# Optimization experiments

Measured on AMD Instinct MI355X. Metric: run time of the kernel, lower is better.

## Reference

```python
import jax, jax.numpy as jnp
import numpy as np

# --- hyperparameters (match module defaults) ---
W_CLASSIFY = 1.1          # weight_factor_classify
W_SAMPLE = 1.0            # weight_factor_sample (mid weight add)
LOSS_WEIGHTS = (1.0, 1.0, 1.0)
PARAMS_HEAD = dict(a=80.0, b=1500.0, c=1750.0, d=2000.0, t=-0.5)
PARAMS_CHEST = dict(a=10.0, b=75.0, c=85.0, d=100.0, t=-0.5)
PARAMS_NECK = dict(a=0.15, b=1.5, c=1.7, d=1.9, t=-0.5)

# AIS thresholds (reimplemented in-kernel; original used numpy round-trips)
HEAD_THR = np.array([150.0, 500.0, 1000.0, 1800.0, 2600.0], dtype=np.float32)
CHEST_THR = np.array([22.0, 35.0, 45.0, 55.0, 65.0], dtype=np.float32)
CHEST_OT_SCALE = np.array([0.8, 0.9, 1.0, 1.1, 1.2], dtype=np.float32)  # per occupant-type
NECK_THR = np.array([0.2, 0.5, 1.0, 1.5, 2.0], dtype=np.float32)


def piecewise_linear(y_true, y_pred, p, mid):
    a, b, c, d, t = p['a'], p['b'], p['c'], p['d'], p['t']
    k = -np.log(t + 1.0) / d  # decay rate for y > d
    w = jnp.zeros_like(y_true)
    w = jnp.where((y_true >= 0) & (y_true < a), (mid / a) * y_true, w)
    w = jnp.where((y_true >= a) & (y_true <= b), mid, w)
    w = jnp.where((y_true > b) & (y_true < c), mid - (mid / (c - b)) * (y_true - b), w)
    w = jnp.where((y_true >= c) & (y_true <= d), 0.0, w)
    w = jnp.where(y_true > d, -1.0 + jnp.exp(-k * (y_true - d)), w)
    w = w + jnp.where(y_pred < 0, mid, 0.0)
    return w


def ais_from_thresholds(x, thr):
    # piecewise-constant AIS class: number of thresholds exceeded, in [0, 5]
    return jnp.sum(x[:, None] >= thr[None, :], axis=-1).astype(jnp.float32)


def task_loss(pred, true, ais_pred, ais_true, params):
    # AIS values are classification results of detached values in the
    # original (no grad) -> stop_gradient here.
    w_cls = W_CLASSIFY ** jnp.abs(jax.lax.stop_gradient(ais_pred) - jax.lax.stop_gradient(ais_true))
    w_mid = 1.0 + piecewise_linear(true, pred, params, W_SAMPLE)
    base = jnp.abs(pred - true)  # MAE, reduction='none'
    return jnp.mean(base * w_cls * w_mid)


def setup_inputs() -> dict:
    key = jax.random.key(0)
    k1, k2, k3 = jax.random.split(key, 3)
    B = 4194304
    scales = jnp.array([2500.0, 120.0, 2.5], dtype=jnp.float32)  # HIC, Dmax, Nij ranges
    pred = (jax.random.uniform(k1, (B, 3), dtype=jnp.float32) * 1.1 - 0.05) * scales
    true = jax.random.uniform(k2, (B, 3), dtype=jnp.float32) * scales
    ot = jax.random.randint(k3, (B,), 0, 5, dtype=jnp.int32)
    return {"pred": pred, "true": true, "ot": ot}


def reference(pred, true, ot):
    thr_head = jnp.asarray(HEAD_THR)
    thr_neck = jnp.asarray(NECK_THR)
    # chest thresholds scale with occupant type -> per-sample thresholds
    thr_chest = jnp.asarray(CHEST_THR)[None, :] * jnp.asarray(CHEST_OT_SCALE)[ot][:, None]

    p_hic, p_dmax, p_nij = pred[:, 0], pred[:, 1], pred[:, 2]
    t_hic, t_dmax, t_nij = true[:, 0], true[:, 1], true[:, 2]

    loss_hic = task_loss(p_hic, t_hic,
                         ais_from_thresholds(p_hic, thr_head),
                         ais_from_thresholds(t_hic, thr_head), PARAMS_HEAD)

    ais_p_chest = jnp.sum(p_dmax[:, None] >= thr_chest, axis=-1).astype(jnp.float32)
    ais_t_chest = jnp.sum(t_dmax[:, None] >= thr_chest, axis=-1).astype(jnp.float32)
    loss_dmax = task_loss(p_dmax, t_dmax, ais_p_chest, ais_t_chest, PARAMS_CHEST)

    loss_nij = task_loss(p_nij, t_nij,
                         ais_from_thresholds(p_nij, thr_neck),
                         ais_from_thresholds(t_nij, thr_neck), PARAMS_NECK)

    w_hic, w_dmax, w_nij = LOSS_WEIGHTS
    return w_hic * loss_hic + w_dmax * loss_dmax + w_nij * loss_nij
```

## Files before the change

### kernel.cpp

```cpp
#include <hip/hip_runtime.h>

#define NT 256
#define NB 1536

__device__ __forceinline__ float elem_loss(float p, float t, float se,
    float t0, float t1, float t2, float t3, float t4,
    float ainv, float bb, float cbinv, float dd, float dinv) {
    float u0 = t0 * se, u1 = t1 * se, u2 = t2 * se, u3 = t3 * se, u4 = t4 * se;
    int ap = (p >= u0) + (p >= u1) + (p >= u2) + (p >= u3) + (p >= u4);
    int at = (t >= u0) + (t >= u1) + (t >= u2) + (t >= u3) + (t >= u4);
    float wc = exp2f(fabsf((float)(ap - at)) * 0.13750352374993502f);
    float ramp = t * ainv;
    float down = 1.0f - (t - bb) * cbinv;
    float wm = fmaxf(fminf(fminf(ramp, 1.0f), down), 0.0f);
    float tail = exp2f((dd - t) * dinv) - 1.0f;
    wm = (t > dd) ? tail : wm;
    wm += (p < 0.0f) ? 2.0f : 1.0f;
    return fabsf(p - t) * wc * wm;
}

#define SEL0(x0, x1, x2) (c1 ? (x1) : (c2 ? (x2) : (x0)))
#define SEL1(x0, x1, x2) (c1 ? (x2) : (c2 ? (x0) : (x1)))
#define SEL2(x0, x1, x2) (c1 ? (x0) : (c2 ? (x1) : (x2)))

#define DECL_SLOT(n, SEL) \
    const float t0_##n = SEL(150.0f, 22.0f, 0.2f); \
    const float t1_##n = SEL(500.0f, 35.0f, 0.5f); \
    const float t2_##n = SEL(1000.0f, 45.0f, 1.0f); \
    const float t3_##n = SEL(1800.0f, 55.0f, 1.5f); \
    const float t4_##n = SEL(2600.0f, 65.0f, 2.0f); \
    const float ainv_##n = SEL(0.0125f, 0.1f, 6.6666667f); \
    const float bb_##n   = SEL(1500.0f, 75.0f, 1.5f); \
    const float cbinv_##n= SEL(0.004f, 0.1f, 5.0f); \
    const float dd_##n   = SEL(2000.0f, 100.0f, 1.9f); \
    const float dinv_##n = SEL(0.0005f, 0.01f, 0.52631579f); \
    const bool  ch_##n   = SEL(false, true, false);

#define SLOT_LOSS(n, p, t) \
    elem_loss((p), (t), ch_##n ? (off_##n ? s1 : s0) : 1.0f, \
              t0_##n, t1_##n, t2_##n, t3_##n, t4_##n, \
              ainv_##n, bb_##n, cbinv_##n, dd_##n, dinv_##n)

__global__ __launch_bounds__(NT)
void weighted_loss_main(const float* __restrict__ pred,
                        const float* __restrict__ truth,
                        const int*   __restrict__ ot,
                        float* __restrict__ partial, int B) {
    const int total  = 3 * B;
    const int nchunk = total >> 2;
    const int g = blockIdx.x * NT + threadIdx.x;
    const int S = gridDim.x * NT;

    const int  q  = g % 3;
    const bool c1 = (q == 1), c2 = (q == 2);

    DECL_SLOT(a, SEL0)
    DECL_SLOT(b, SEL1)
    DECL_SLOT(c, SEL2)

    const bool off_a = false;
    const bool off_b = c2;
    const bool off_c = c1 || c2;
    const bool off_d = true;

    const float4* p4 = (const float4*)pred;
    const float4* t4 = (const float4*)truth;

    float acc = 0.0f;
    for (int C = g; C < nchunk; C += S) {
        float4 pv = p4[C];
        float4 tv = t4[C];
        unsigned r0 = (unsigned)(((4u * (unsigned)C - (unsigned)q) * 0xAAAAAAABull) >> 33);
        int o0 = ot[r0];
        int o1 = ot[r0 + 1];
        float s0 = fmaf(0.1f, (float)o0, 0.8f);
        float s1 = fmaf(0.1f, (float)o1, 0.8f);

        acc += SLOT_LOSS(a, pv.x, tv.x);
        acc += SLOT_LOSS(b, pv.y, tv.y);
        acc += SLOT_LOSS(c, pv.z, tv.z);
        acc += elem_loss(pv.w, tv.w, ch_a ? (off_d ? s1 : s0) : 1.0f,
                         t0_a, t1_a, t2_a, t3_a, t4_a,
                         ainv_a, bb_a, cbinv_a, dd_a, dinv_a);
        (void)off_a;
    }

    for (int idx = (nchunk << 2) + g; idx < total; idx += S) {
        int role = idx % 3, row = idx / 3;
        float p = pred[idx], t = truth[idx];
        float l;
        if (role == 0)
            l = elem_loss(p, t, 1.0f, 150.0f, 500.0f, 1000.0f, 1800.0f, 2600.0f,
                          0.0125f, 1500.0f, 0.004f, 2000.0f, 0.0005f);
        else if (role == 1)
            l = elem_loss(p, t, fmaf(0.1f, (float)ot[row], 0.8f),
                          22.0f, 35.0f, 45.0f, 55.0f, 65.0f,
                          0.1f, 75.0f, 0.1f, 100.0f, 0.01f);
        else
            l = elem_loss(p, t, 1.0f, 0.2f, 0.5f, 1.0f, 1.5f, 2.0f,
                          6.6666667f, 1.5f, 5.0f, 1.9f, 0.52631579f);
        acc += l;
    }

    #pragma unroll
    for (int off = 32; off > 0; off >>= 1) acc += __shfl_down(acc, off, 64);
    __shared__ float sm[NT / 64];
    const int lane = threadIdx.x & 63, wid = threadIdx.x >> 6;
    if (lane == 0) sm[wid] = acc;
    __syncthreads();
    if (threadIdx.x == 0) {
        float s = 0.0f;
        #pragma unroll
        for (int w = 0; w < NT / 64; ++w) s += sm[w];
        partial[blockIdx.x] = s;
    }
}

__global__ __launch_bounds__(256)
void weighted_loss_reduce(const float* __restrict__ partial, int n,
                          float* __restrict__ out, float invB) {
    float acc = 0.0f;
    for (int i = threadIdx.x; i < n; i += blockDim.x) acc += partial[i];
    #pragma unroll
    for (int off = 32; off > 0; off >>= 1) acc += __shfl_down(acc, off, 64);
    __shared__ float sm[4];
    const int lane = threadIdx.x & 63, wid = threadIdx.x >> 6;
    if (lane == 0) sm[wid] = acc;
    __syncthreads();
    if (threadIdx.x == 0)
        out[0] = (sm[0] + sm[1] + sm[2] + sm[3]) * invB;
}

extern "C" void kernel_launch(void* const* d_in, const int* in_sizes, int n_in,
                              void* d_out, int out_size, void* d_ws, size_t ws_size,
                              hipStream_t stream) {
    const float* pred  = (const float*)d_in[0];
    const float* truth = (const float*)d_in[1];
    const int*   ot    = (const int*)d_in[2];
    const int B = in_sizes[2];
    float* partial = (float*)d_ws;

    weighted_loss_main<<<NB, NT, 0, stream>>>(pred, truth, ot, partial, B);
    weighted_loss_reduce<<<1, 256, 0, stream>>>(partial, NB, (float*)d_out,
                                                1.0f / (float)B);
}
```

Measured before the change: 138.4 us.

## Issue four chunk loads per thread up front with doubled grid

Doubles the grid so that four times the total thread count equals the number of float4 chunks at this problem size. A specialized path then issues all four chunks' pred, truth and occupant-type loads before doing any arithmetic, so more memory requests are in flight per thread. A generic strided loop remains as a fallback for other sizes. The final reduce kernel is widened to 1024 threads to handle the larger number of partial sums.

```diff
diff --git a/kernel.cpp b/kernel.cpp
--- a/kernel.cpp
+++ b/kernel.cpp
@@ -1,7 +1,7 @@
 #include <hip/hip_runtime.h>
 
 #define NT 256
-#define NB 1536
+#define NB 3072
 
 __device__ __forceinline__ float elem_loss(float p, float t, float se,
     float t0, float t1, float t2, float t3, float t4,
@@ -36,8 +36,8 @@
     const float dinv_##n = SEL(0.0005f, 0.01f, 0.52631579f); \
     const bool  ch_##n   = SEL(false, true, false);
 
-#define SLOT_LOSS(n, p, t) \
-    elem_loss((p), (t), ch_##n ? (off_##n ? s1 : s0) : 1.0f, \
+#define SLOT_LOSS(n, p, t, s0, s1) \
+    elem_loss((p), (t), ch_##n ? (off_##n ? (s1) : (s0)) : 1.0f, \
               t0_##n, t1_##n, t2_##n, t3_##n, t4_##n, \
               ainv_##n, bb_##n, cbinv_##n, dd_##n, dinv_##n)
 
@@ -61,45 +61,65 @@
     const bool off_a = false;
     const bool off_b = c2;
     const bool off_c = c1 || c2;
-    const bool off_d = true;
 
     const float4* p4 = (const float4*)pred;
     const float4* t4 = (const float4*)truth;
 
     float acc = 0.0f;
-    for (int C = g; C < nchunk; C += S) {
-        float4 pv = p4[C];
-        float4 tv = t4[C];
-        unsigned r0 = (unsigned)(((4u * (unsigned)C - (unsigned)q) * 0xAAAAAAABull) >> 33);
-        int o0 = ot[r0];
-        int o1 = ot[r0 + 1];
-        float s0 = fmaf(0.1f, (float)o0, 0.8f);
-        float s1 = fmaf(0.1f, (float)o1, 0.8f);
 
-        acc += SLOT_LOSS(a, pv.x, tv.x);
-        acc += SLOT_LOSS(b, pv.y, tv.y);
-        acc += SLOT_LOSS(c, pv.z, tv.z);
-        acc += elem_loss(pv.w, tv.w, ch_a ? (off_d ? s1 : s0) : 1.0f,
-                         t0_a, t1_a, t2_a, t3_a, t4_a,
-                         ainv_a, bb_a, cbinv_a, dd_a, dinv_a);
-        (void)off_a;
-    }
-
-    for (int idx = (nchunk << 2) + g; idx < total; idx += S) {
-        int role = idx % 3, row = idx / 3;
-        float p = pred[idx], t = truth[idx];
-        float l;
-        if (role == 0)
-            l = elem_loss(p, t, 1.0f, 150.0f, 500.0f, 1000.0f, 1800.0f, 2600.0f,
-                          0.0125f, 1500.0f, 0.004f, 2000.0f, 0.0005f);
-        else if (role == 1)
-            l = elem_loss(p, t, fmaf(0.1f, (float)ot[row], 0.8f),
-                          22.0f, 35.0f, 45.0f, 55.0f, 65.0f,
-                          0.1f, 75.0f, 0.1f, 100.0f, 0.01f);
-        else
-            l = elem_loss(p, t, 1.0f, 0.2f, 0.5f, 1.0f, 1.5f, 2.0f,
-                          6.6666667f, 1.5f, 5.0f, 1.9f, 0.52631579f);
-        acc += l;
+    if (nchunk == (S << 2)) {
+        float4 pv[4], tv[4];
+        int    o0[4], o1[4];
+        #pragma unroll
+        for (int k = 0; k < 4; ++k) {
+            const int C = g + k * S;
+            pv[k] = p4[C];
+            tv[k] = t4[C];
+            unsigned r0 = (unsigned)(((4u * (unsigned)C - (unsigned)q)
+                                      * 0xAAAAAAABull) >> 33);
+            o0[k] = ot[r0];
+            o1[k] = ot[r0 + 1];
+        }
+        #pragma unroll
+        for (int k = 0; k < 4; ++k) {
+            float s0 = fmaf(0.1f, (float)o0[k], 0.8f);
+            float s1 = fmaf(0.1f, (float)o1[k], 0.8f);
+            acc += SLOT_LOSS(a, pv[k].x, tv[k].x, s0, s1);
+            acc += SLOT_LOSS(b, pv[k].y, tv[k].y, s0, s1);
+            acc += SLOT_LOSS(c, pv[k].z, tv[k].z, s0, s1);
+            acc += elem_loss(pv[k].w, tv[k].w, ch_a ? s1 : 1.0f,
+                             t0_a, t1_a, t2_a, t3_a, t4_a,
+                             ainv_a, bb_a, cbinv_a, dd_a, dinv_a);
+        }
+    } else {
+        for (int C = g; C < nchunk; C += S) {
+            float4 pv = p4[C];
+            float4 tv = t4[C];
+            unsigned r0 = (unsigned)(((4u * (unsigned)C - (unsigned)q)
+                                      * 0xAAAAAAABull) >> 33);
+            float s0 = fmaf(0.1f, (float)ot[r0], 0.8f);
+            float s1 = fmaf(0.1f, (float)ot[r0 + 1], 0.8f);
+            acc += SLOT_LOSS(a, pv.x, tv.x, s0, s1);
+            acc += SLOT_LOSS(b, pv.y, tv.y, s0, s1);
+            acc += SLOT_LOSS(c, pv.z, tv.z, s0, s1);
+            acc += elem_loss(pv.w, tv.w, ch_a ? s1 : 1.0f,
+                             t0_a, t1_a, t2_a, t3_a, t4_a,
+                             ainv_a, bb_a, cbinv_a, dd_a, dinv_a);
+        }
+        for (int idx = (nchunk << 2) + g; idx < total; idx += S) {
+            int role = idx % 3, row = idx / 3;
+            float p = pred[idx], t = truth[idx];
+            if (role == 0)
+                acc += elem_loss(p, t, 1.0f, 150.0f, 500.0f, 1000.0f, 1800.0f, 2600.0f,
+                                 0.0125f, 1500.0f, 0.004f, 2000.0f, 0.0005f);
+            else if (role == 1)
+                acc += elem_loss(p, t, fmaf(0.1f, (float)ot[row], 0.8f),
+                                 22.0f, 35.0f, 45.0f, 55.0f, 65.0f,
+                                 0.1f, 75.0f, 0.1f, 100.0f, 0.01f);
+            else
+                acc += elem_loss(p, t, 1.0f, 0.2f, 0.5f, 1.0f, 1.5f, 2.0f,
+                                 6.6666667f, 1.5f, 5.0f, 1.9f, 0.52631579f);
+        }
     }
 
     #pragma unroll
@@ -116,19 +136,23 @@
     }
 }
 
-__global__ __launch_bounds__(256)
+__global__ __launch_bounds__(1024)
 void weighted_loss_reduce(const float* __restrict__ partial, int n,
                           float* __restrict__ out, float invB) {
     float acc = 0.0f;
     for (int i = threadIdx.x; i < n; i += blockDim.x) acc += partial[i];
     #pragma unroll
     for (int off = 32; off > 0; off >>= 1) acc += __shfl_down(acc, off, 64);
-    __shared__ float sm[4];
+    __shared__ float sm[16];
     const int lane = threadIdx.x & 63, wid = threadIdx.x >> 6;
     if (lane == 0) sm[wid] = acc;
     __syncthreads();
-    if (threadIdx.x == 0)
-        out[0] = (sm[0] + sm[1] + sm[2] + sm[3]) * invB;
+    if (threadIdx.x == 0) {
+        float s = 0.0f;
+        #pragma unroll
+        for (int w = 0; w < 16; ++w) s += sm[w];
+        out[0] = s * invB;
+    }
 }
 
 extern "C" void kernel_launch(void* const* d_in, const int* in_sizes, int n_in,
@@ -141,6 +165,6 @@
     float* partial = (float*)d_ws;
 
     weighted_loss_main<<<NB, NT, 0, stream>>>(pred, truth, ot, partial, B);
-    weighted_loss_reduce<<<1, 256, 0, stream>>>(partial, NB, (float*)d_out,
-                                                1.0f / (float)B);
+    weighted_loss_reduce<<<1, 1024, 0, stream>>>(partial, NB, (float*)d_out,
+                                                 1.0f / (float)B);
 }
```

Result: no change. 137.6 us (-0.5%).
